# Performance work log

Hardware: AMD Instinct MI355X
Metric: run time of the kernel (lower is better)

The kernel has to match this reference:

```python
import jax, jax.numpy as jnp
import numpy as np
import math

B, E, N = 32, 256, 64
KV_DIM, Q_DIM = 100, 768


def setup_inputs() -> dict:
    key = jax.random.key(0)
    ks = jax.random.split(key, 8)
    q = jax.random.normal(ks[0], (B, Q_DIM), dtype=jnp.float32)
    k = jax.random.normal(ks[1], (B, E, N, KV_DIM), dtype=jnp.float32)
    v = jax.random.normal(ks[2], (B, E, N, KV_DIM), dtype=jnp.float32)
    input_ent = jax.random.randint(ks[3], (B, E), 0, 50000)
    # xavier-uniform-initialized weights (torch Linear: y = x @ W.T + b)
    def xavier(k_, fan_out, fan_in):
        lim = math.sqrt(6.0 / (fan_in + fan_out))
        return jax.random.uniform(k_, (fan_out, fan_in), jnp.float32, -lim, lim)
    W_q = xavier(ks[4], KV_DIM, Q_DIM)
    b_q = jnp.zeros((KV_DIM,), jnp.float32)
    W_kv = xavier(ks[5], KV_DIM, KV_DIM)
    W_v = xavier(ks[6], KV_DIM, KV_DIM)
    return {"input_ent": input_ent, "q": q, "k": k, "v": v,
            "W_q": W_q, "b_q": b_q, "W_kv": W_kv, "W_v": W_v}


def reference(input_ent, q, k, v, W_q, b_q, W_kv, W_v):
    # mode == 'candidate_pos', graphsage=False -> output = self_attention(q, k, v)
    # Q projection + tanh: [B, Kv]
    Qp = jnp.tanh(q @ W_q.T + b_q)
    # K projection: [B, E, N, Kv]
    Kp = k @ W_kv.T
    # broadcasted dot-product score: [B, E, N]
    att = jnp.einsum('bd,bend->ben', Qp, Kp) / math.sqrt(KV_DIM)
    # masked_fill(att == 0, -10000)
    att = jnp.where(att == 0.0, jnp.float32(-10000.0), att)
    # LeakyReLU (default negative_slope=0.01) then softmax over neighbor dim
    att = jax.nn.softmax(jax.nn.leaky_relu(att, 0.01), axis=2)
    # masked_fill(att == 1/N, 0)
    att = jnp.where(att == jnp.float32(1.0 / N), jnp.float32(0.0), att)
    # V projection and weighted aggregation over neighbors: [B, E, Kv]
    Vp = v @ W_v.T
    return jnp.einsum('ben,bend->bed', att, Vp)
```

## Files before the change

### kernel.cpp

```cpp
#include <hip/hip_runtime.h>

#define B 32
#define E 256
#define N 64
#define KV 100
#define QD 768
#define NF4 ((N * KV) / 4)

typedef float floatx4 __attribute__((ext_vector_type(4)));

#define ASYNC16(gsrc, ldst) \
    __builtin_amdgcn_global_load_lds( \
        (const __attribute__((address_space(1))) void*)(gsrc), \
        (__attribute__((address_space(3))) void*)(ldst), 16, 0, 0)

__device__ __forceinline__ float dot4f(float4 a, float4 b) {
    return a.x * b.x + a.y * b.y + a.z * b.z + a.w * b.w;
}

__device__ __forceinline__ float4 ntload4(const float4* p) {
    floatx4 r = __builtin_nontemporal_load((const floatx4*)p);
    return make_float4(r.x, r.y, r.z, r.w);
}

__global__ __launch_bounds__(256) void prep_kernel(
    const float* __restrict__ q, const float* __restrict__ W_q,
    const float* __restrict__ b_q, const float* __restrict__ W_kv,
    float* __restrict__ Qk)
{
    const int tid = threadIdx.x;
    const int b   = blockIdx.x;

    __shared__ float q_lds[QD];
    __shared__ float Qp_lds[KV];

    for (int i = tid; i < QD; i += 256) q_lds[i] = q[b * QD + i];
    __syncthreads();

    const int i = tid >> 1, h = tid & 1;
    if (i < KV) {
        float acc = 0.f;
        const float* wrow = W_q + i * QD + h * (QD / 2);
        const float* qrow = q_lds + h * (QD / 2);
        #pragma unroll 8
        for (int d = 0; d < QD / 2; d++) acc += qrow[d] * wrow[d];
        acc += __shfl_xor(acc, 1);
        if (h == 0) Qp_lds[i] = tanhf(acc + b_q[i]);
    }
    __syncthreads();

    if (tid < KV) {
        float acc = 0.f;
        #pragma unroll 4
        for (int ii = 0; ii < KV; ii++) acc += Qp_lds[ii] * W_kv[ii * KV + tid];
        Qk[b * KV + tid] = acc * 0.1f;
    }
}

__global__ __launch_bounds__(256, 4) void attn_kernel(
    const float* __restrict__ k,
    const float* __restrict__ v,
    const float* __restrict__ Qk,
    float* __restrict__ agg_out)
{
    __shared__ __align__(16) float vbuf[N * KV];
    __shared__ float kpbuf[NF4];
    __shared__ __align__(16) float qk_lds[4][KV];
    __shared__ float att_lds[N];

    const int tid  = threadIdx.x;
    const int wid  = tid >> 6;
    const int lane = tid & 63;
    const int be   = blockIdx.x;
    const int b    = be >> 8;

    const float4* kb4 = (const float4*)(k + (size_t)be * (N * KV));
    const float4* vb4 = (const float4*)(v + (size_t)be * (N * KV));
    float4* vbuf4 = (float4*)vbuf;

    float4 qkreg = make_float4(0.f, 0.f, 0.f, 0.f);
    if (lane < KV / 4) qkreg = ((const float4*)(Qk + b * KV))[lane];

    float4 kk[7];
    #pragma unroll
    for (int r = 0; r < 7; r++) {
        int f = r * 256 + tid; if (f > NF4 - 1) f = NF4 - 1;
        kk[r] = ntload4(kb4 + f);
    }

    #pragma unroll
    for (int i = 0; i < 6; i++)
        ASYNC16(vb4 + i * 256 + tid, vbuf4 + i * 256 + (tid & 192));
    if (tid < 64) ASYNC16(vb4 + 1536 + tid, vbuf4 + 1536);

    if (lane < KV / 4) ((float4*)qk_lds[wid])[lane] = qkreg;

    int c = tid % 25;
    #pragma unroll
    for (int r = 0; r < 7; r++) {
        int f = r * 256 + tid;
        if (f < NF4) {
            float4 qq = ((const float4*)qk_lds[wid])[c];
            kpbuf[f] = dot4f(kk[r], qq);
        }
        c += 6; if (c >= 25) c -= 25;
    }
    __syncthreads();

    if (tid < N) {
        float s = 0.f;
        #pragma unroll
        for (int j = 0; j < 25; j++) s += kpbuf[tid * 25 + j];
        if (s == 0.0f) s = -10000.0f;
        s = (s > 0.0f) ? s : 0.01f * s;
        float m = s;
        #pragma unroll
        for (int o = 32; o; o >>= 1) m = fmaxf(m, __shfl_xor(m, o));
        float e = __expf(s - m);
        float su = e;
        #pragma unroll
        for (int o = 32; o; o >>= 1) su += __shfl_xor(su, o);
        float r = e / su;
        if (r == 0.015625f) r = 0.f;
        att_lds[tid] = r;
    }
    __syncthreads();

    if (tid < KV) {
        float a = 0.f;
        #pragma unroll 8
        for (int n = 0; n < N; n++)
            a += att_lds[n] * vbuf[n * KV + tid];
        agg_out[(size_t)be * KV + tid] = a;
    }
}

__global__ __launch_bounds__(256) void proj_kernel(
    const float* __restrict__ agg,
    const float* __restrict__ W_v,
    float* __restrict__ out)
{
    __shared__ __align__(16) float a_lds[4][KV];
    const int tid = threadIdx.x, wid = tid >> 6, lane = tid & 63;
    const int be  = blockIdx.x * 4 + wid;

    if (lane < 25)
        ((float4*)a_lds[wid])[lane] = ((const float4*)(agg + (size_t)be * KV))[lane];

    const float4* wv4 = (const float4*)W_v;
    const float4* a4  = (const float4*)a_lds[wid];
    #pragma unroll
    for (int p = 0; p < 2; p++) {
        const int i = p * 64 + lane;
        if (i < KV) {
            float acc = 0.f;
            #pragma unroll
            for (int j = 0; j < 25; j++) acc += dot4f(wv4[i * 25 + j], a4[j]);
            out[(size_t)be * KV + i] = acc;
        }
    }
}

extern "C" void kernel_launch(void* const* d_in, const int* in_sizes, int n_in,
                              void* d_out, int out_size, void* d_ws, size_t ws_size,
                              hipStream_t stream) {
    const float* q    = (const float*)d_in[1];
    const float* k    = (const float*)d_in[2];
    const float* v    = (const float*)d_in[3];
    const float* W_q  = (const float*)d_in[4];
    const float* b_q  = (const float*)d_in[5];
    const float* W_kv = (const float*)d_in[6];
    const float* W_v  = (const float*)d_in[7];
    float* out  = (float*)d_out;

    float* Qk  = (float*)d_ws;
    float* agg = Qk + B * KV;

    prep_kernel<<<B, 256, 0, stream>>>(q, W_q, b_q, W_kv, Qk);
    attn_kernel<<<B * E, 256, 0, stream>>>(k, v, Qk, agg);
    proj_kernel<<<(B * E) / 4, 256, 0, stream>>>(agg, W_v, out);
}
```

Baseline: 109.2 us.

## Fuse V projection into attention kernel and remap block order across XCDs

Removes the separate projection kernel: each attention block now keeps the aggregated vector in LDS and multiplies it by W_v directly, writing the final output. This drops one kernel launch and the round trip of the intermediate buffer through global memory. The block index is also permuted so that consecutive hardware blocks map to entries spread in a strided pattern, likely aimed at XCD/L2 locality. The cost is an extra barrier and W_v reads inside every attention block.

```diff
diff --git a/kernel.cpp b/kernel.cpp
--- a/kernel.cpp
+++ b/kernel.cpp
@@ -61,17 +61,20 @@
     const float* __restrict__ k,
     const float* __restrict__ v,
     const float* __restrict__ Qk,
-    float* __restrict__ agg_out)
+    const float* __restrict__ W_v,
+    float* __restrict__ out)
 {
     __shared__ __align__(16) float vbuf[N * KV];
     __shared__ float kpbuf[NF4];
     __shared__ __align__(16) float qk_lds[4][KV];
     __shared__ float att_lds[N];
+    __shared__ __align__(16) float agg_lds[KV];
 
     const int tid  = threadIdx.x;
     const int wid  = tid >> 6;
     const int lane = tid & 63;
-    const int be   = blockIdx.x;
+    const int orig = blockIdx.x;
+    const int be   = ((orig & 7) << 10) | (orig >> 3);
     const int b    = be >> 8;
 
     const float4* kb4 = (const float4*)(k + (size_t)be * (N * KV));
@@ -131,33 +134,23 @@
         #pragma unroll 8
         for (int n = 0; n < N; n++)
             a += att_lds[n] * vbuf[n * KV + tid];
-        agg_out[(size_t)be * KV + tid] = a;
+        agg_lds[tid] = a;
     }
-}
+    __syncthreads();
 
-__global__ __launch_bounds__(256) void proj_kernel(
-    const float* __restrict__ agg,
-    const float* __restrict__ W_v,
-    float* __restrict__ out)
-{
-    __shared__ __align__(16) float a_lds[4][KV];
-    const int tid = threadIdx.x, wid = tid >> 6, lane = tid & 63;
-    const int be  = blockIdx.x * 4 + wid;
-
-    if (lane < 25)
-        ((float4*)a_lds[wid])[lane] = ((const float4*)(agg + (size_t)be * KV))[lane];
-
-    const float4* wv4 = (const float4*)W_v;
-    const float4* a4  = (const float4*)a_lds[wid];
-    #pragma unroll
-    for (int p = 0; p < 2; p++) {
-        const int i = p * 64 + lane;
-        if (i < KV) {
-            float acc = 0.f;
-            #pragma unroll
-            for (int j = 0; j < 25; j++) acc += dot4f(wv4[i * 25 + j], a4[j]);
-            out[(size_t)be * KV + i] = acc;
+    const int p = tid >> 1, h = tid & 1;
+    if (p < KV) {
+        const float4* wrow = (const float4*)(W_v + p * KV);
+        const float4* a4   = (const float4*)agg_lds;
+        float acc = 0.f;
+        #pragma unroll
+        for (int j = h; j < KV / 4; j += 2) {
+            float4 w = wrow[j];
+            float4 a = a4[j];
+            acc += w.x * a.x + w.y * a.y + w.z * a.z + w.w * a.w;
         }
+        acc += __shfl_xor(acc, 1);
+        if (h == 0) out[(size_t)be * KV + p] = acc;
     }
 }
 
@@ -173,10 +166,8 @@
     const float* W_v  = (const float*)d_in[7];
     float* out  = (float*)d_out;
 
-    float* Qk  = (float*)d_ws;
-    float* agg = Qk + B * KV;
+    float* Qk = (float*)d_ws;
 
     prep_kernel<<<B, 256, 0, stream>>>(q, W_q, b_q, W_kv, Qk);
-    attn_kernel<<<B * E, 256, 0, stream>>>(k, v, Qk, agg);
-    proj_kernel<<<(B * E) / 4, 256, 0, stream>>>(agg, W_v, out);
+    attn_kernel<<<B * E, 256, 0, stream>>>(k, v, Qk, W_v, out);
 }
```

Result: faster. 101.6 us (-7.0%).
